# Performance work log

Measured on AMD Instinct MI355X. Metric: run time of the kernel, lower is better.

The kernel has to match this reference:

```python
import jax, jax.numpy as jnp
import numpy as np

B, S, D, H, HID = 4, 1024, 1024, 16, 4096
DK = D // H
EPS = 1e-6


def _ln(x):
    # LayerNorm without affine, eps=1e-6
    mu = jnp.mean(x, axis=-1, keepdims=True)
    var = jnp.var(x, axis=-1, keepdims=True)
    return (x - mu) / jnp.sqrt(var + EPS)


def _lin(x, W, b):
    # torch Linear convention: W is [out, in]
    y = jnp.einsum('...i,oi->...o', x, W)
    return y + b if b is not None else y


def setup_inputs() -> dict:
    key = jax.random.key(0)
    ks = jax.random.split(key, 16)
    sc = lambda fan_in: 1.0 / np.sqrt(fan_in)
    inp = {
        'x': jax.random.normal(ks[0], (B, S, D), jnp.float32),
        'cond': jax.random.normal(ks[1], (B, 1, D), jnp.float32),
        'Wq': jax.random.normal(ks[2], (D, D), jnp.float32) * sc(D),
        'bq': jnp.zeros((D,), jnp.float32),
        'Wk': jax.random.normal(ks[3], (D, D), jnp.float32) * sc(D),
        'bk': jnp.zeros((D,), jnp.float32),
        'Wv': jax.random.normal(ks[4], (D, D), jnp.float32) * sc(D),
        'bv': jnp.zeros((D,), jnp.float32),
        'Wo': jax.random.normal(ks[5], (D, D), jnp.float32) * sc(D),
        'bo': jnp.zeros((D,), jnp.float32),
        'W1': jax.random.normal(ks[6], (HID, D), jnp.float32) * sc(D),
        'b1': jnp.zeros((HID,), jnp.float32),
        'W2': jax.random.normal(ks[7], (D, HID), jnp.float32) * sc(HID),
        'b2': jnp.zeros((D,), jnp.float32),
        'Wada': jax.random.normal(ks[8], (6 * D, D), jnp.float32) * sc(D),
        'bada': jnp.zeros((6 * D,), jnp.float32),
    }
    return inp


def reference(x, cond, Wq, bq, Wk, bk, Wv, bv, Wo, bo, W1, b1, W2, b2, Wada, bada):
    # adaLN modulation: SiLU -> Linear -> chunk 6 along last dim
    mod = _lin(jax.nn.silu(cond), Wada, bada)  # [B,1,6D]
    gama1, beta1, alpha1, gama2, beta2, alpha2 = jnp.split(mod, 6, axis=-1)

    # attention branch
    residual = x
    h = _ln(x) * (1.0 + beta1) + gama1  # modulate(shift=gama1, scale=beta1)
    q = _lin(h, Wq, bq).reshape(B, S, H, DK)
    k = _lin(h, Wk, bk).reshape(B, S, H, DK)
    v = _lin(h, Wv, bv).reshape(B, S, H, DK)
    scores = jnp.einsum('bqhd,bkhd->bhqk', q, k) / jnp.sqrt(jnp.float32(DK))
    probs = jax.nn.softmax(scores, axis=-1)
    attn = jnp.einsum('bhqk,bkhd->bqhd', probs, v).reshape(B, S, D)
    attn = _lin(attn, Wo, bo)
    x = residual + alpha1 * attn

    # MLP branch
    residual = x
    h = _ln(x) * (1.0 + beta2) + gama2
    h = _lin(h, W1, b1)
    h = jax.nn.gelu(h, approximate=False)  # torch nn.GELU default (erf)
    h = _lin(h, W2, b2)
    return residual + alpha2 * h
```

## Files before the change

### kernel.cpp

```cpp
#include <hip/hip_runtime.h>
#include <cstdint>

typedef __bf16 bf16_t;
typedef __bf16 bf16x4 __attribute__((ext_vector_type(4)));
typedef __bf16 bf16x8 __attribute__((ext_vector_type(8)));
typedef float f32x4 __attribute__((ext_vector_type(4)));

#define B_ 4
#define S_ 1024
#define D_ 1024
#define HID_ 4096
#define MEG (1u << 20)

static const size_t OFF_WBF  = 0;
static const size_t OFF_BQKV = 25165824;
static const size_t OFF_MOD  = 25178112;
static const size_t OFF_H    = 25276416;
static const size_t OFF_QKV  = 33665024;
static const size_t OFF_VT   = 58830848;
static const size_t OFF_ATTN = 67219456;
static const size_t OFF_X1   = 75608064;
static const size_t OFF_PART = 92385280;
static const size_t OFF_MLPH = 159494144;

__device__ __forceinline__ void async_copy16(const bf16_t* g, bf16_t* l) {
  __builtin_amdgcn_global_load_lds(
      (__attribute__((address_space(1))) void*)(g),
      (__attribute__((address_space(3))) void*)(l), 16, 0, 0);
}

__global__ __launch_bounds__(256) void convert_pack(
    const float* __restrict__ Wq, const float* __restrict__ Wk,
    const float* __restrict__ Wv, const float* __restrict__ Wo,
    const float* __restrict__ W1, const float* __restrict__ W2,
    const float* __restrict__ bq, const float* __restrict__ bk,
    const float* __restrict__ bv, bf16_t* __restrict__ wbf,
    float* __restrict__ bqkv) {
  const int y = blockIdx.y;
  if (y == 6) {
    int i = blockIdx.x * 256 + threadIdx.x;
    if (i < 3072)
      bqkv[i] = i < 1024 ? bq[i] : (i < 2048 ? bk[i - 1024] : bv[i - 2048]);
    return;
  }
  const float* src; bf16_t* dst; int n;
  switch (y) {
    case 0: src = Wq; dst = wbf;           n = MEG;     break;
    case 1: src = Wk; dst = wbf + MEG;     n = MEG;     break;
    case 2: src = Wv; dst = wbf + 2*MEG;   n = MEG;     break;
    case 3: src = Wo; dst = wbf + 3*MEG;   n = MEG;     break;
    case 4: src = W1; dst = wbf + 4*MEG;   n = 4*MEG;   break;
    default: src = W2; dst = wbf + 8*MEG;  n = 4*MEG;   break;
  }
  int idx = (blockIdx.x * 256 + threadIdx.x) * 4;
  if (idx < n) {
    float4 v = *(const float4*)(src + idx);
    bf16x4 pk;
    pk.x = (__bf16)v.x; pk.y = (__bf16)v.y; pk.z = (__bf16)v.z; pk.w = (__bf16)v.w;
    *(bf16x4*)(dst + idx) = pk;
  }
}

__global__ __launch_bounds__(256) void ada_mod(
    const float* __restrict__ cond, const float* __restrict__ Wada,
    const float* __restrict__ bada, float* __restrict__ mod) {
  const int wave = threadIdx.x >> 6, lane = threadIdx.x & 63;
  const int o = blockIdx.x * 4 + wave;
  const float* wr = Wada + (size_t)o * D_;
  float a0 = 0.f, a1 = 0.f, a2 = 0.f, a3 = 0.f;
#pragma unroll
  for (int l = 0; l < 16; l++) {
    int i = l * 64 + lane;
    float w = wr[i];
    float c0 = cond[i], c1 = cond[1024 + i], c2 = cond[2048 + i], c3 = cond[3072 + i];
    a0 += w * (c0 / (1.0f + __expf(-c0)));
    a1 += w * (c1 / (1.0f + __expf(-c1)));
    a2 += w * (c2 / (1.0f + __expf(-c2)));
    a3 += w * (c3 / (1.0f + __expf(-c3)));
  }
#pragma unroll
  for (int offs = 32; offs; offs >>= 1) {
    a0 += __shfl_xor(a0, offs);
    a1 += __shfl_xor(a1, offs);
    a2 += __shfl_xor(a2, offs);
    a3 += __shfl_xor(a3, offs);
  }
  if (lane == 0) {
    float bb = bada[o];
    mod[o]          = a0 + bb;
    mod[6144 + o]   = a1 + bb;
    mod[12288 + o]  = a2 + bb;
    mod[18432 + o]  = a3 + bb;
  }
}

__global__ __launch_bounds__(256) void ln_modulate(
    const float* __restrict__ X, const float* __restrict__ mod,
    bf16_t* __restrict__ H, int goff) {
  const int row = blockIdx.x;
  const int b = row >> 10;
  const int t = threadIdx.x;
  const float* xr = X + (size_t)row * D_;
  float4 xv = *(const float4*)(xr + t * 4);
  float s = xv.x + xv.y + xv.z + xv.w;
  float q = xv.x*xv.x + xv.y*xv.y + xv.z*xv.z + xv.w*xv.w;
  const int wave = t >> 6, lane = t & 63;
#pragma unroll
  for (int offs = 32; offs; offs >>= 1) {
    s += __shfl_down(s, offs);
    q += __shfl_down(q, offs);
  }
  __shared__ float sb[4][2];
  if (lane == 0) { sb[wave][0] = s; sb[wave][1] = q; }
  __syncthreads();
  float st = sb[0][0] + sb[1][0] + sb[2][0] + sb[3][0];
  float qt = sb[0][1] + sb[1][1] + sb[2][1] + sb[3][1];
  float mu = st * (1.0f / D_);
  float var = qt * (1.0f / D_) - mu * mu;
  float rstd = rsqrtf(var + 1e-6f);
  const float* mb = mod + (size_t)b * 6144 + goff;
  const int c = t * 4;
  float4 gm = *(const float4*)(mb + c);
  float4 bt = *(const float4*)(mb + 1024 + c);
  bf16x4 pk;
  pk.x = (__bf16)((xv.x - mu) * rstd * (1.0f + bt.x) + gm.x);
  pk.y = (__bf16)((xv.y - mu) * rstd * (1.0f + bt.y) + gm.y);
  pk.z = (__bf16)((xv.z - mu) * rstd * (1.0f + bt.z) + gm.z);
  pk.w = (__bf16)((xv.w - mu) * rstd * (1.0f + bt.w) + gm.w);
  *(bf16x4*)(H + (size_t)row * D_ + c) = pk;
}

__global__ __launch_bounds__(256) void transpose_v(
    const bf16_t* __restrict__ qkv, bf16_t* __restrict__ vT) {
  __shared__ bf16_t tile[64][65];
  const int bh = blockIdx.y;
  const int b = bh >> 4, hh = bh & 15;
  const int s0 = blockIdx.x * 64;
  const int t = threadIdx.x;
  const int tx = t & 63, ty = t >> 6;
  const bf16_t* src = qkv + (size_t)b * S_ * 3072 + 2048 + hh * 64;
  for (int r = ty; r < 64; r += 4)
    tile[r][tx] = src[(size_t)(s0 + r) * 3072 + tx];
  __syncthreads();
  bf16_t* dst = vT + (size_t)bh * 64 * 1024;
  for (int r = ty; r < 64; r += 4)
    dst[(size_t)r * 1024 + s0 + tx] = tile[tx][r];
}

__global__ __launch_bounds__(512, 4) void flash_attn(
    const bf16_t* __restrict__ qkv, const bf16_t* __restrict__ vT,
    bf16_t* __restrict__ attn) {
  __shared__ __align__(16) bf16_t Ks[2][2][64 * 64];
  __shared__ __align__(16) bf16_t Vs[2][2][64 * 64];
  __shared__ __align__(16) bf16_t Ps[8][16 * 64];

  const int t = threadIdx.x;
  const int wave = t >> 6, lane = t & 63;
  const int lm = lane & 15, quad = lane >> 4;
  const int bh = blockIdx.y;
  const int b = bh >> 4, hh = bh & 15;
  const int s0 = blockIdx.x * 128;

  const bf16_t* qbase = qkv + (size_t)b * S_ * 3072 + hh * 64;
  const bf16_t* kbase = qbase + 1024;
  const bf16_t* vbase = vT + (size_t)bh * (64 * 1024);

  const int row0 = t >> 3;
  const int cg = (t & 7) ^ (row0 & 7);
  const int od = t * 8;

  async_copy16(qbase + (size_t)(s0 + row0) * 3072 + cg * 8, &Ks[1][0][od]);
  async_copy16(qbase + (size_t)(s0 + 64 + row0) * 3072 + cg * 8, &Ks[1][1][od]);
  async_copy16(kbase + (size_t)row0 * 3072 + cg * 8, &Ks[0][0][od]);
  async_copy16(kbase + (size_t)(64 + row0) * 3072 + cg * 8, &Ks[0][1][od]);
  async_copy16(vbase + (size_t)row0 * 1024 + cg * 8, &Vs[0][0][od]);
  async_copy16(vbase + (size_t)row0 * 1024 + 64 + cg * 8, &Vs[0][1][od]);
  __syncthreads();

  bf16x8 aq0, aq1;
  {
    const int rq = wave * 16 + lm;
    const int qh = rq >> 6, qr = rq & 63;
    const int rbq = lm & 7;
    aq0 = *(const bf16x8*)&Ks[1][qh][qr * 64 + (quad ^ rbq) * 8];
    aq1 = *(const bf16x8*)&Ks[1][qh][qr * 64 + ((4 + quad) ^ rbq) * 8];
  }
  __syncthreads();

  f32x4 accO[4] = {};
  float mrow[4], lsum[4];
#pragma unroll
  for (int r = 0; r < 4; r++) { mrow[r] = -1e30f; lsum[r] = 0.f; }

  const float SC = 0.18033688f;
  const int rb = lm & 7;
  bf16_t* Pw = Ps[wave];

  for (int tt = 0; tt < 8; ++tt) {
    const int cur = tt & 1;
    if (tt < 7) {
      const int nb = cur ^ 1;
      const size_t k0n = (size_t)(tt + 1) << 7;
      async_copy16(kbase + (k0n + row0) * 3072 + cg * 8, &Ks[nb][0][od]);
      async_copy16(kbase + (k0n + 64 + row0) * 3072 + cg * 8, &Ks[nb][1][od]);
      async_copy16(vbase + (size_t)row0 * 1024 + k0n + cg * 8, &Vs[nb][0][od]);
      async_copy16(vbase + (size_t)row0 * 1024 + k0n + 64 + cg * 8, &Vs[nb][1][od]);
    }

    f32x4 accS[8];
#pragma unroll
    for (int j = 0; j < 8; j++) accS[j] = (f32x4){0.f, 0.f, 0.f, 0.f};
    __builtin_amdgcn_s_setprio(1);
#pragma unroll
    for (int hf = 0; hf < 2; hf++) {
#pragma unroll
      for (int ni = 0; ni < 4; ni++) {
        const int rk = ni * 16 + lm;
        bf16x8 b0 = *(const bf16x8*)&Ks[cur][hf][rk * 64 + ((quad ^ rb)) * 8];
        bf16x8 b1 = *(const bf16x8*)&Ks[cur][hf][rk * 64 + (((4 + quad) ^ rb)) * 8];
        f32x4 a = accS[hf * 4 + ni];
        a = __builtin_amdgcn_mfma_f32_16x16x32_bf16(aq0, b0, a, 0, 0, 0);
        a = __builtin_amdgcn_mfma_f32_16x16x32_bf16(aq1, b1, a, 0, 0, 0);
        accS[hf * 4 + ni] = a;
      }
    }
    __builtin_amdgcn_s_setprio(0);

    float mx[4];
#pragma unroll
    for (int r = 0; r < 4; r++) {
      float m0 = fmaxf(fmaxf(accS[0][r], accS[1][r]), fmaxf(accS[2][r], accS[3][r]));
      float m1 = fmaxf(fmaxf(accS[4][r], accS[5][r]), fmaxf(accS[6][r], accS[7][r]));
      float m8 = fmaxf(m0, m1);
      m8 = fmaxf(m8, __shfl_xor(m8, 1));
      m8 = fmaxf(m8, __shfl_xor(m8, 2));
      m8 = fmaxf(m8, __shfl_xor(m8, 4));
      m8 = fmaxf(m8, __shfl_xor(m8, 8));
      mx[r] = m8 * SC;
    }
    bool ok = (mx[0] - mrow[0] <= 8.0f) && (mx[1] - mrow[1] <= 8.0f) &&
              (mx[2] - mrow[2] <= 8.0f) && (mx[3] - mrow[3] <= 8.0f);
    if (!__all(ok)) {
#pragma unroll
      for (int r = 0; r < 4; r++) {
        float mnew = fmaxf(mrow[r], mx[r]);
        float al = exp2f(mrow[r] - mnew);
        mrow[r] = mnew;
        lsum[r] *= al;
#pragma unroll
        for (int di = 0; di < 4; di++) accO[di][r] *= al;
      }
    }
#pragma unroll
    for (int r = 0; r < 4; r++) {
      float sum = 0.f;
#pragma unroll
      for (int j = 0; j < 8; j++) {
        float p = exp2f(accS[j][r] * SC - mrow[r]);
        accS[j][r] = p;
        sum += p;
      }
      lsum[r] += sum;
    }

#pragma unroll
    for (int hf = 0; hf < 2; hf++) {
#pragma unroll
      for (int jj = 0; jj < 4; jj++)
#pragma unroll
        for (int r = 0; r < 4; r++) {
          int prow = quad * 4 + r;
          int c = jj * 16 + lm;
          Pw[prow * 64 + (((c >> 3) ^ (prow & 7)) << 3) + (c & 7)] =
              (__bf16)accS[hf * 4 + jj][r];
        }
      __builtin_amdgcn_s_setprio(1);
#pragma unroll
      for (int loc = 0; loc < 2; loc++) {
        bf16x8 ap = *(const bf16x8*)&Pw[lm * 64 + (((loc * 4 + quad) ^ rb)) * 8];
#pragma unroll
        for (int di = 0; di < 4; di++) {
          const int rv = di * 16 + lm;
          bf16x8 vv = *(const bf16x8*)&Vs[cur][hf]
              [rv * 64 + (((loc * 4 + quad) ^ rb)) * 8];
          accO[di] = __builtin_amdgcn_mfma_f32_16x16x32_bf16(ap, vv, accO[di], 0, 0, 0);
        }
      }
      __builtin_amdgcn_s_setprio(0);
    }
    __syncthreads();
  }

#pragma unroll
  for (int r = 0; r < 4; r++) {
    float sv = lsum[r];
    sv += __shfl_xor(sv, 1);
    sv += __shfl_xor(sv, 2);
    sv += __shfl_xor(sv, 4);
    sv += __shfl_xor(sv, 8);
    lsum[r] = sv;
  }

#pragma unroll
  for (int r = 0; r < 4; r++) {
    float inv = 1.0f / lsum[r];
    int prow = quad * 4 + r;
#pragma unroll
    for (int di = 0; di < 4; di++) {
      int col = di * 16 + lm;
      int cph = (col >> 3) ^ (prow & 7);
      Pw[prow * 64 + cph * 8 + (col & 7)] = (__bf16)(accO[di][r] * inv);
    }
  }
  bf16_t* abase = attn + (size_t)b * S_ * 1024 +
                  (size_t)(s0 + wave * 16) * 1024 + hh * 64;
#pragma unroll
  for (int it = 0; it < 2; it++) {
    int slot = it * 64 + lane;
    int orow = slot >> 3;
    int gc = slot & 7;
    int cph = gc ^ (orow & 7);
    bf16x8 val = *(const bf16x8*)&Pw[orow * 64 + cph * 8];
    *(bf16x8*)(abase + (size_t)orow * 1024 + gc * 8) = val;
  }
}

template <int EPI>
__global__ __launch_bounds__(256) void gemm_bt(
    const bf16_t* __restrict__ A, int lda, long long sAz,
    const bf16_t* __restrict__ B, int ldb, long long sBz,
    void* __restrict__ Cv, int ldc, long long sCz,
    int M, int N, int K,
    const float* __restrict__ bias,
    float scale) {
  __shared__ __align__(16) bf16_t As[3][128 * 32];
  __shared__ __align__(16) bf16_t Bs[3][128 * 32];

  const int z = blockIdx.z;
  A += (size_t)z * sAz;
  B += (size_t)z * sBz;

  {
    int d = blockIdx.x + gridDim.x * blockIdx.y;
    int xcd = d & 7, sId = d >> 3;
    int qq = sId & 31, panel = sId >> 5;
    const int bx = panel * 8 + (qq >> 2);
    const int by = xcd * 4 + (qq & 3);
    const int t = threadIdx.x;
    const int wave = t >> 6;
    const int lane = t & 63;
    const int lm = lane & 15;
    const int quad = lane >> 4;
    const int wr = wave >> 1;
    const int wc = wave & 1;

    const int m0 = by * 128;
    const int n0 = bx * 128;

    f32x4 acc[4][4] = {};

    const int srow = t >> 2;
    const int gch = (t & 3) ^ ((srow >> 1) & 3);
    const int lds_off = t * 8;
    const bf16_t* Ap0 = A + (size_t)(m0 + srow) * lda + gch * 8;
    const bf16_t* Ap1 = A + (size_t)(m0 + 64 + srow) * lda + gch * 8;
    const bf16_t* Bp0 = B + (size_t)(n0 + srow) * ldb + gch * 8;
    const bf16_t* Bp1 = B + (size_t)(n0 + 64 + srow) * ldb + gch * 8;

    const int sOff = (quad ^ ((lm >> 1) & 3)) * 8;

    const int niter = K >> 5;
    async_copy16(Ap0, &As[0][lds_off]);
    async_copy16(Ap1, &As[0][2048 + lds_off]);
    async_copy16(Bp0, &Bs[0][lds_off]);
    async_copy16(Bp1, &Bs[0][2048 + lds_off]);
    if (niter > 1) {
      async_copy16(Ap0 + 32, &As[1][lds_off]);
      async_copy16(Ap1 + 32, &As[1][2048 + lds_off]);
      async_copy16(Bp0 + 32, &Bs[1][lds_off]);
      async_copy16(Bp1 + 32, &Bs[1][2048 + lds_off]);
    }

    int cur = 0;
    for (int it = 0; it < niter; ++it) {
      if (it + 1 < niter) {
        asm volatile("s_waitcnt vmcnt(4)\n\ts_barrier" ::: "memory");
      } else {
        asm volatile("s_waitcnt vmcnt(0)\n\ts_barrier" ::: "memory");
      }
      if (it + 2 < niter) {
        const int ko = (it + 2) << 5;
        const int nb = (cur >= 1) ? cur - 1 : 2;
        async_copy16(Ap0 + ko, &As[nb][lds_off]);
        async_copy16(Ap1 + ko, &As[nb][2048 + lds_off]);
        async_copy16(Bp0 + ko, &Bs[nb][lds_off]);
        async_copy16(Bp1 + ko, &Bs[nb][2048 + lds_off]);
      }
      bf16x8 af[4], bfr[4];
#pragma unroll
      for (int i = 0; i < 4; i++) {
        af[i] = *(const bf16x8*)&As[cur][(wr * 64 + i * 16 + lm) * 32 + sOff];
        bfr[i] = *(const bf16x8*)&Bs[cur][(wc * 64 + i * 16 + lm) * 32 + sOff];
      }
#pragma unroll
      for (int mi = 0; mi < 4; mi++)
#pragma unroll
        for (int ni = 0; ni < 4; ni++)
          acc[mi][ni] = __builtin_amdgcn_mfma_f32_16x16x32_bf16(
              af[mi], bfr[ni], acc[mi][ni], 0, 0, 0);
      cur = (cur == 2) ? 0 : cur + 1;
    }

    const size_t cz = (size_t)z * sCz;
#pragma unroll
    for (int mi = 0; mi < 4; mi++) {
#pragma unroll
      for (int ni = 0; ni < 4; ni++) {
#pragma unroll
        for (int r = 0; r < 4; r++) {
          int row = m0 + wr * 64 + mi * 16 + quad * 4 + r;
          int col = n0 + wc * 64 + ni * 16 + lm;
          float v = acc[mi][ni][r];
          size_t idx = cz + (size_t)row * ldc + col;
          if (EPI == 1) {
            ((float*)Cv)[idx] = v * scale;
          } else if (EPI == 0) {
            if (bias) v += bias[col];
            ((bf16_t*)Cv)[idx] = (__bf16)v;
          } else if (EPI == 3) {
            v += bias[col];
            float u = 1.5957691216f * (v + 0.044715f * v * v * v);
            float g = v / (1.0f + __expf(-u));
            ((bf16_t*)Cv)[idx] = (__bf16)g;
          }
        }
      }
    }
  }
}

__global__ __launch_bounds__(256) void reduce_ln(
    const float* __restrict__ part, const float* __restrict__ x,
    const float* __restrict__ bo, const float* __restrict__ mod,
    float* __restrict__ x1, bf16_t* __restrict__ h) {
  const int row = blockIdx.x;
  const int b = row >> 10;
  const int t = threadIdx.x;
  const int c = t * 4;
  const size_t idx = (size_t)row * 1024 + c;
  float4 p0 = *(const float4*)(part + idx);
  float4 p1 = *(const float4*)(part + 4194304 + idx);
  float4 bb = *(const float4*)(bo + c);
  float4 al = *(const float4*)(mod + (size_t)b * 6144 + 2048 + c);
  float4 xs = *(const float4*)(x + idx);
  float4 xv;
  xv.x = xs.x + al.x * (p0.x + p1.x + bb.x);
  xv.y = xs.y + al.y * (p0.y + p1.y + bb.y);
  xv.z = xs.z + al.z * (p0.z + p1.z + bb.z);
  xv.w = xs.w + al.w * (p0.w + p1.w + bb.w);
  *(float4*)(x1 + idx) = xv;

  float s = xv.x + xv.y + xv.z + xv.w;
  float q = xv.x*xv.x + xv.y*xv.y + xv.z*xv.z + xv.w*xv.w;
  const int wave = t >> 6, lane = t & 63;
#pragma unroll
  for (int offs = 32; offs; offs >>= 1) {
    s += __shfl_down(s, offs);
    q += __shfl_down(q, offs);
  }
  __shared__ float sb[4][2];
  if (lane == 0) { sb[wave][0] = s; sb[wave][1] = q; }
  __syncthreads();
  float st = sb[0][0] + sb[1][0] + sb[2][0] + sb[3][0];
  float qt = sb[0][1] + sb[1][1] + sb[2][1] + sb[3][1];
  float mu = st * (1.0f / D_);
  float var = qt * (1.0f / D_) - mu * mu;
  float rstd = rsqrtf(var + 1e-6f);
  const float* mb = mod + (size_t)b * 6144 + 3072;
  float4 gm = *(const float4*)(mb + c);
  float4 bt = *(const float4*)(mb + 1024 + c);
  bf16x4 pk;
  pk.x = (__bf16)((xv.x - mu) * rstd * (1.0f + bt.x) + gm.x);
  pk.y = (__bf16)((xv.y - mu) * rstd * (1.0f + bt.y) + gm.y);
  pk.z = (__bf16)((xv.z - mu) * rstd * (1.0f + bt.z) + gm.z);
  pk.w = (__bf16)((xv.w - mu) * rstd * (1.0f + bt.w) + gm.w);
  *(bf16x4*)(h + idx) = pk;
}

__global__ __launch_bounds__(256) void reduce_w2(
    const float* __restrict__ part, const float* __restrict__ x1,
    const float* __restrict__ b2, const float* __restrict__ mod,
    float* __restrict__ out) {
  const int idx = (blockIdx.x * 256 + threadIdx.x) * 4;
  const int col = idx & 1023;
  const int row = idx >> 10;
  const int b = row >> 10;
  float4 s0 = *(const float4*)(part + idx);
  float4 s1 = *(const float4*)(part + 4194304 + idx);
  float4 bb = *(const float4*)(b2 + col);
  float4 al = *(const float4*)(mod + (size_t)b * 6144 + 5120 + col);
  float4 rs = *(const float4*)(x1 + idx);
  float4 o;
  o.x = rs.x + al.x * (s0.x + s1.x + bb.x);
  o.y = rs.y + al.y * (s0.y + s1.y + bb.y);
  o.z = rs.z + al.z * (s0.z + s1.z + bb.z);
  o.w = rs.w + al.w * (s0.w + s1.w + bb.w);
  *(float4*)(out + idx) = o;
}

extern "C" void kernel_launch(void* const* d_in, const int* in_sizes, int n_in,
                              void* d_out, int out_size, void* d_ws, size_t ws_size,
                              hipStream_t stream) {
  (void)in_sizes; (void)n_in; (void)out_size; (void)ws_size;
  const float* x    = (const float*)d_in[0];
  const float* cond = (const float*)d_in[1];
  const float* Wq   = (const float*)d_in[2];
  const float* bq   = (const float*)d_in[3];
  const float* Wk   = (const float*)d_in[4];
  const float* bk   = (const float*)d_in[5];
  const float* Wv   = (const float*)d_in[6];
  const float* bv   = (const float*)d_in[7];
  const float* Wo   = (const float*)d_in[8];
  const float* bo   = (const float*)d_in[9];
  const float* W1   = (const float*)d_in[10];
  const float* b1   = (const float*)d_in[11];
  const float* W2   = (const float*)d_in[12];
  const float* b2   = (const float*)d_in[13];
  const float* Wada = (const float*)d_in[14];
  const float* bada = (const float*)d_in[15];

  uint8_t* ws = (uint8_t*)d_ws;
  bf16_t* wbf   = (bf16_t*)(ws + OFF_WBF);
  float*  bqkv  = (float*)(ws + OFF_BQKV);
  float*  mod   = (float*)(ws + OFF_MOD);
  bf16_t* h     = (bf16_t*)(ws + OFF_H);
  bf16_t* qkv   = (bf16_t*)(ws + OFF_QKV);
  bf16_t* vT    = (bf16_t*)(ws + OFF_VT);
  bf16_t* attn  = (bf16_t*)(ws + OFF_ATTN);
  float*  x1    = (float*)(ws + OFF_X1);
  float*  part  = (float*)(ws + OFF_PART);
  bf16_t* mlph  = (bf16_t*)(ws + OFF_MLPH);
  float* out = (float*)d_out;

  convert_pack<<<dim3(4096, 7, 1), 256, 0, stream>>>(Wq, Wk, Wv, Wo, W1, W2,
                                                     bq, bk, bv, wbf, bqkv);
  ada_mod<<<1536, 256, 0, stream>>>(cond, Wada, bada, mod);
  ln_modulate<<<4096, 256, 0, stream>>>(x, mod, h, 0);
  gemm_bt<0><<<dim3(24, 32, 1), 256, 0, stream>>>(
      h, 1024, 0, wbf, 1024, 0, qkv, 3072, 0, 4096, 3072, 1024,
      bqkv, 1.f);
  transpose_v<<<dim3(16, 64, 1), 256, 0, stream>>>(qkv, vT);
  flash_attn<<<dim3(8, 64, 1), 512, 0, stream>>>(qkv, vT, attn);

  gemm_bt<1><<<dim3(8, 32, 2), 256, 0, stream>>>(
      attn, 1024, 512, wbf + (size_t)3 * MEG, 1024, 512, part, 1024, 4194304,
      4096, 1024, 512, nullptr, 1.f);
  reduce_ln<<<4096, 256, 0, stream>>>(part, x, bo, mod, x1, h);

  gemm_bt<3><<<dim3(32, 32, 1), 256, 0, stream>>>(
      h, 1024, 0, wbf + (size_t)4 * MEG, 1024, 0, mlph, 4096, 0,
      4096, 4096, 1024, b1, 1.f);
  gemm_bt<1><<<dim3(8, 32, 2), 256, 0, stream>>>(
      mlph, 4096, 2048, wbf + (size_t)8 * MEG, 4096, 2048, part, 1024, 4194304,
      4096, 1024, 2048, nullptr, 1.f);
  reduce_w2<<<4096, 256, 0, stream>>>(part, x1, b2, mod, out);
}
```

Measured before the change: 399.0 us.

## Enlarge GEMM tiles to 256x128 with 512 threads and BK=64

The GEMM kernel moves from 128x128 tiles with 4 waves and a K step of 32 to 256x128 tiles with 8 waves and a K step of 64. The LDS swizzle is changed to match, the XCD-aware block remap is replaced by a generic chunked mapping, and the MFMA loop is wrapped in s_setprio. The goal is more reuse of each B tile, fewer barriers per unit of K, and less global traffic. In exchange, LDS use rises to about 144KB per block, which limits occupancy to one block per CU, and the grids shrink, which can cause wave-quantization tail effects on 256 CUs.

New measurement: 412.5 us. +3.4%, slower.

```diff
diff --git a/kernel.cpp b/kernel.cpp
--- a/kernel.cpp
+++ b/kernel.cpp
@@ -326,26 +326,28 @@
 }
 
 template <int EPI>
-__global__ __launch_bounds__(256) void gemm_bt(
+__global__ __launch_bounds__(512) void gemm_bt(
     const bf16_t* __restrict__ A, int lda, long long sAz,
     const bf16_t* __restrict__ B, int ldb, long long sBz,
     void* __restrict__ Cv, int ldc, long long sCz,
     int M, int N, int K,
     const float* __restrict__ bias,
     float scale) {
-  __shared__ __align__(16) bf16_t As[3][128 * 32];
-  __shared__ __align__(16) bf16_t Bs[3][128 * 32];
+  __shared__ __align__(16) bf16_t As[3][256 * 64];
+  __shared__ __align__(16) bf16_t Bs[3][128 * 64];
 
   const int z = blockIdx.z;
   A += (size_t)z * sAz;
   B += (size_t)z * sBz;
 
+  const int gx = gridDim.x;
+  int d = blockIdx.x + gx * blockIdx.y;
   {
-    int d = blockIdx.x + gridDim.x * blockIdx.y;
-    int xcd = d & 7, sId = d >> 3;
-    int qq = sId & 31, panel = sId >> 5;
-    const int bx = panel * 8 + (qq >> 2);
-    const int by = xcd * 4 + (qq & 3);
+    const int cpx = (gx * gridDim.y) >> 3;
+    int wg = (d & 7) * cpx + (d >> 3);
+    const int by = wg / gx;
+    const int bx = wg % gx;
+
     const int t = threadIdx.x;
     const int wave = t >> 6;
     const int lane = t & 63;
@@ -354,62 +356,70 @@
     const int wr = wave >> 1;
     const int wc = wave & 1;
 
-    const int m0 = by * 128;
+    const int m0 = by * 256;
     const int n0 = bx * 128;
 
     f32x4 acc[4][4] = {};
 
-    const int srow = t >> 2;
-    const int gch = (t & 3) ^ ((srow >> 1) & 3);
-    const int lds_off = t * 8;
-    const bf16_t* Ap0 = A + (size_t)(m0 + srow) * lda + gch * 8;
-    const bf16_t* Ap1 = A + (size_t)(m0 + 64 + srow) * lda + gch * 8;
-    const bf16_t* Bp0 = B + (size_t)(n0 + srow) * ldb + gch * 8;
-    const bf16_t* Bp1 = B + (size_t)(n0 + 64 + srow) * ldb + gch * 8;
-
-    const int sOff = (quad ^ ((lm >> 1) & 3)) * 8;
-
-    const int niter = K >> 5;
-    async_copy16(Ap0, &As[0][lds_off]);
-    async_copy16(Ap1, &As[0][2048 + lds_off]);
-    async_copy16(Bp0, &Bs[0][lds_off]);
-    async_copy16(Bp1, &Bs[0][2048 + lds_off]);
-    if (niter > 1) {
-      async_copy16(Ap0 + 32, &As[1][lds_off]);
-      async_copy16(Ap1 + 32, &As[1][2048 + lds_off]);
-      async_copy16(Bp0 + 32, &Bs[1][lds_off]);
-      async_copy16(Bp1 + 32, &Bs[1][2048 + lds_off]);
-    }
+    const int srow = t >> 3;
+    const int scg = (t & 7) ^ (srow & 7);
+    const int sod = t * 8;
+    const bf16_t* Ag = A + (size_t)(m0 + srow) * lda + scg * 8;
+    const bf16_t* Bg = B + (size_t)(n0 + srow) * ldb + scg * 8;
+    const size_t a64 = (size_t)64 * lda, a128 = (size_t)128 * lda,
+                 a192 = (size_t)192 * lda, b64 = (size_t)64 * ldb;
+
+#define STAGE6(buf, ko)                                      \
+  async_copy16(Ag + (ko), &As[buf][sod]);                    \
+  async_copy16(Ag + a64 + (ko), &As[buf][4096 + sod]);       \
+  async_copy16(Ag + a128 + (ko), &As[buf][8192 + sod]);      \
+  async_copy16(Ag + a192 + (ko), &As[buf][12288 + sod]);     \
+  async_copy16(Bg + (ko), &Bs[buf][sod]);                    \
+  async_copy16(Bg + b64 + (ko), &Bs[buf][4096 + sod]);
+
+    const int niter = K >> 6;
+    STAGE6(0, 0);
+    STAGE6(1, 64);
+
+    const int rbx = lm & 7;
+    const int sl0 = (quad ^ rbx) * 8;
+    const int sl1 = ((4 + quad) ^ rbx) * 8;
+    const int arow = wr * 4096 + lm * 64;
+    const int brow = wc * 4096 + lm * 64;
 
     int cur = 0;
     for (int it = 0; it < niter; ++it) {
       if (it + 1 < niter) {
-        asm volatile("s_waitcnt vmcnt(4)\n\ts_barrier" ::: "memory");
+        asm volatile("s_waitcnt vmcnt(6)\n\ts_barrier" ::: "memory");
       } else {
         asm volatile("s_waitcnt vmcnt(0)\n\ts_barrier" ::: "memory");
       }
       if (it + 2 < niter) {
-        const int ko = (it + 2) << 5;
         const int nb = (cur >= 1) ? cur - 1 : 2;
-        async_copy16(Ap0 + ko, &As[nb][lds_off]);
-        async_copy16(Ap1 + ko, &As[nb][2048 + lds_off]);
-        async_copy16(Bp0 + ko, &Bs[nb][lds_off]);
-        async_copy16(Bp1 + ko, &Bs[nb][2048 + lds_off]);
-      }
-      bf16x8 af[4], bfr[4];
+        const int ko = (it + 2) << 6;
+        STAGE6(nb, ko);
+      }
+      bf16x8 af[4][2], bfr[4][2];
 #pragma unroll
       for (int i = 0; i < 4; i++) {
-        af[i] = *(const bf16x8*)&As[cur][(wr * 64 + i * 16 + lm) * 32 + sOff];
-        bfr[i] = *(const bf16x8*)&Bs[cur][(wc * 64 + i * 16 + lm) * 32 + sOff];
-      }
-#pragma unroll
-      for (int mi = 0; mi < 4; mi++)
-#pragma unroll
-        for (int ni = 0; ni < 4; ni++)
-          acc[mi][ni] = __builtin_amdgcn_mfma_f32_16x16x32_bf16(
-              af[mi], bfr[ni], acc[mi][ni], 0, 0, 0);
+        af[i][0] = *(const bf16x8*)&As[cur][arow + i * 1024 + sl0];
+        af[i][1] = *(const bf16x8*)&As[cur][arow + i * 1024 + sl1];
+        bfr[i][0] = *(const bf16x8*)&Bs[cur][brow + i * 1024 + sl0];
+        bfr[i][1] = *(const bf16x8*)&Bs[cur][brow + i * 1024 + sl1];
+      }
+      __builtin_amdgcn_s_setprio(1);
+#pragma unroll
+      for (int ks = 0; ks < 2; ks++)
+#pragma unroll
+        for (int mi = 0; mi < 4; mi++)
+#pragma unroll
+          for (int ni = 0; ni < 4; ni++)
+            acc[mi][ni] = __builtin_amdgcn_mfma_f32_16x16x32_bf16(
+                af[mi][ks], bfr[ni][ks], acc[mi][ni], 0, 0, 0);
+      __builtin_amdgcn_s_setprio(0);
       cur = (cur == 2) ? 0 : cur + 1;
     }
+#undef STAGE6
 
     const size_t cz = (size_t)z * sCz;
 #pragma unroll
@@ -546,21 +556,21 @@
                                                      bq, bk, bv, wbf, bqkv);
   ada_mod<<<1536, 256, 0, stream>>>(cond, Wada, bada, mod);
   ln_modulate<<<4096, 256, 0, stream>>>(x, mod, h, 0);
-  gemm_bt<0><<<dim3(24, 32, 1), 256, 0, stream>>>(
+  gemm_bt<0><<<dim3(24, 16, 1), 512, 0, stream>>>(
       h, 1024, 0, wbf, 1024, 0, qkv, 3072, 0, 4096, 3072, 1024,
       bqkv, 1.f);
   transpose_v<<<dim3(16, 64, 1), 256, 0, stream>>>(qkv, vT);
   flash_attn<<<dim3(8, 64, 1), 512, 0, stream>>>(qkv, vT, attn);
 
-  gemm_bt<1><<<dim3(8, 32, 2), 256, 0, stream>>>(
+  gemm_bt<1><<<dim3(8, 16, 2), 512, 0, stream>>>(
       attn, 1024, 512, wbf + (size_t)3 * MEG, 1024, 512, part, 1024, 4194304,
       4096, 1024, 512, nullptr, 1.f);
   reduce_ln<<<4096, 256, 0, stream>>>(part, x, bo, mod, x1, h);
 
-  gemm_bt<3><<<dim3(32, 32, 1), 256, 0, stream>>>(
+  gemm_bt<3><<<dim3(32, 16, 1), 512, 0, stream>>>(
       h, 1024, 0, wbf + (size_t)4 * MEG, 1024, 0, mlph, 4096, 0,
       4096, 4096, 1024, b1, 1.f);
-  gemm_bt<1><<<dim3(8, 32, 2), 256, 0, stream>>>(
+  gemm_bt<1><<<dim3(8, 16, 2), 512, 0, stream>>>(
       mlph, 4096, 2048, wbf + (size_t)8 * MEG, 4096, 2048, part, 1024, 4194304,
       4096, 1024, 2048, nullptr, 1.f);
   reduce_w2<<<4096, 256, 0, stream>>>(part, x1, b2, mod, out);
```
